# Kernel tuning notes

Hardware: AMD Instinct MI355X
Metric: run time of the kernel (lower is better)

## Reference

```python
import jax, jax.numpy as jnp
import numpy as np

B, L, D_IN, H, C = 64, 2048, 400, 200, 32
NEG = 1e12


def setup_inputs() -> dict:
    key = jax.random.key(0)
    k1, k2, k3, k4, k5 = jax.random.split(key, 5)
    x = jax.random.normal(k1, (B, L, D_IN), dtype=jnp.float32)
    category_bias = jax.random.normal(k2, (B, L, C), dtype=jnp.float32)
    att_mask = (jax.random.uniform(k3, (B, L)) > 0.2).astype(jnp.float32)
    # glorot-uniform-ish scales
    W_proj = jax.random.normal(k4, (D_IN, H), dtype=jnp.float32) * np.float32(np.sqrt(2.0 / (D_IN + H)))
    context = jax.random.normal(k5, (C, H), dtype=jnp.float32) * np.float32(np.sqrt(2.0 / (C + H)))
    lamada = jnp.zeros((1,), dtype=jnp.float32)
    return {"x": x, "category_bias": category_bias, "att_mask": att_mask,
            "W_proj": W_proj, "context": context, "lamada": lamada}


def reference(x, category_bias, att_mask, W_proj, context, lamada):
    # proj: [B, L, H] = tanh(x @ W_proj)  (Dense, no bias)
    proj = jnp.tanh(jnp.einsum("bld,dh->blh", x, W_proj))
    # scores vs learned context vectors: [B, L, C]
    weights = jnp.einsum("blh,ch->blc", proj, context) + lamada * category_bias
    # [B, C, L]
    weights = jnp.transpose(weights, (0, 2, 1))
    # additive large-negative mask, then softmax over sequence
    weights = weights - (1.0 - att_mask[:, None, :]) * NEG
    weights = jax.nn.softmax(weights, axis=-1)
    # poly representation: [B, C, D_IN]
    return jnp.einsum("bcl,bld->bcd", weights, x)
```

## Files before the change

kernel.cpp:

```cpp
#include <hip/hip_runtime.h>
#include <cmath>
#include <cstdint>

#define B_ 64
#define L_ 2048
#define DIN 400
#define H_ 200
#define C_ 32
#define NEGBIG 1e12f
#define KC1 13
#define NT1 13
#define KC2 7
#define MT2 2
#define NLC 16

typedef _Float16 half8 __attribute__((ext_vector_type(8)));
typedef float f32x4 __attribute__((ext_vector_type(4)));
typedef unsigned int uint4v __attribute__((ext_vector_type(4)));

__device__ __align__(16) _Float16 g_wfrag[KC1 * NT1 * 512];
__device__ __align__(16) _Float16 g_cfrag[KC2 * MT2 * 512];

static __device__ __forceinline__ f32x4 mfma16(half8 a, half8 b, f32x4 c) {
  return __builtin_amdgcn_mfma_f32_16x16x32_f16(a, b, c, 0, 0, 0);
}

static __device__ __forceinline__ float fast_tanh(float v) {
  const float e = __expf(2.0f * v);
  return 1.0f - 2.0f / (e + 1.0f);
}

__global__ __launch_bounds__(64) void k_prep(const float* __restrict__ Wp,
                                             const float* __restrict__ ctx)
{
  const int lane = threadIdx.x;
  const int bid = blockIdx.x;
  if (bid < KC1 * NT1) {
    const int q = bid / NT1, nt = bid % NT1;
    const int kb = q * 32 + (lane >> 4) * 8;
    const int n  = nt * 16 + (lane & 15);
    half8 h;
#pragma unroll
    for (int j = 0; j < 8; ++j) {
      const int k = kb + j;
      const float v = (k < DIN && n < H_) ? Wp[(size_t)k * H_ + n] : 0.0f;
      h[j] = (_Float16)v;
    }
    *reinterpret_cast<half8*>(&g_wfrag[((size_t)bid << 9) + (lane << 3)]) = h;
  } else {
    const int r = bid - KC1 * NT1;
    const int c  = (r % MT2) * 16 + (lane & 15);
    const int hb = (r / MT2) * 32 + (lane >> 4) * 8;
    half8 h;
#pragma unroll
    for (int j = 0; j < 8; ++j) {
      const int hh = hb + j;
      const float v = (hh < H_) ? ctx[(size_t)c * H_ + hh] : 0.0f;
      h[j] = (_Float16)v;
    }
    *reinterpret_cast<half8*>(&g_cfrag[((size_t)r << 9) + (lane << 3)]) = h;
  }
}

__global__ __launch_bounds__(256, 5) void k_scores(
    const float* __restrict__ x,
    const float* __restrict__ cb,
    const float* __restrict__ mask,
    const float* __restrict__ lam,
    float* __restrict__ S)
{
  __shared__ half8 smemv[1792];

  const int tid  = threadIdx.x;
  const int lane = tid & 63;
  const int w    = __builtin_amdgcn_readfirstlane(tid >> 6);
  const int b    = blockIdx.y;
  const int l0   = blockIdx.x * 64;
  const int oct  = lane >> 4;

  f32x4 acc[NT1];
#pragma unroll
  for (int nt = 0; nt < NT1; ++nt) acc[nt] = f32x4{0.f, 0.f, 0.f, 0.f};

  const float* xrow =
      x + ((size_t)b * L_ + l0 + w * 16 + (lane & 15)) * DIN + oct * 8;

  for (int i = w; i < NT1; i += 4) {
    const _Float16* gp = g_wfrag + (((size_t)i) << 9) + (lane << 3);
    __builtin_amdgcn_global_load_lds(
        (const __attribute__((address_space(1))) void*)gp,
        (__attribute__((address_space(3))) void*)(smemv + i * 64),
        16, 0, 0);
  }
  __builtin_amdgcn_sched_barrier(0);
  float4 cur0 = *reinterpret_cast<const float4*>(xrow);
  float4 cur1 = *reinterpret_cast<const float4*>(xrow + 4);

#pragma unroll
  for (int q = 0; q < KC1; ++q) {
    asm volatile("s_waitcnt vmcnt(2)\n\ts_barrier" ::: "memory");

    float4 nx0 = float4{0.f, 0.f, 0.f, 0.f};
    float4 nx1 = float4{0.f, 0.f, 0.f, 0.f};
    if (q < KC1 - 1) {
      const int nb = ((q + 1) & 1) * 832;
      for (int i = w; i < NT1; i += 4) {
        const _Float16* gp =
            g_wfrag + (((size_t)((q + 1) * NT1 + i)) << 9) + (lane << 3);
        __builtin_amdgcn_global_load_lds(
            (const __attribute__((address_space(1))) void*)gp,
            (__attribute__((address_space(3))) void*)(smemv + nb + i * 64),
            16, 0, 0);
      }
      __builtin_amdgcn_sched_barrier(0);
      const int k0 = (q + 1) * 32 + oct * 8;
      if (k0 + 7 < DIN) {
        nx0 = *reinterpret_cast<const float4*>(xrow + (q + 1) * 32);
        nx1 = *reinterpret_cast<const float4*>(xrow + (q + 1) * 32 + 4);
      }
    }

    float fa[8] = {cur0.x, cur0.y, cur0.z, cur0.w,
                   cur1.x, cur1.y, cur1.z, cur1.w};
    half8 ah;
#pragma unroll
    for (int j = 0; j < 8; ++j) ah[j] = (_Float16)fa[j];

    const int base = (q & 1) * 832;
#pragma unroll
    for (int nt = 0; nt < NT1; ++nt) {
      const half8 bh = smemv[base + nt * 64 + lane];
      acc[nt] = mfma16(ah, bh, acc[nt]);
    }
    cur0 = nx0;
    cur1 = nx1;
  }

  __syncthreads();
  if (lane >= 32) {
    half8 z = {};
    smemv[(24 + w) * 64 + lane] = z;
  }
  _Float16* Pp = reinterpret_cast<_Float16*>(smemv);
#pragma unroll
  for (int nt = 0; nt < NT1; ++nt) {
    const int h   = nt * 16 + (lane & 15);
    const int q2  = h >> 5;
    const int lpw = ((h >> 3) & 3) << 4;
    const int jj  = h & 7;
#pragma unroll
    for (int reg = 0; reg < 4; ++reg) {
      const int t = ((lane >> 4) << 2) + reg;
      const float p = fast_tanh(acc[nt][reg]);
      Pp[(size_t)(((q2 * 4 + w) * 64) + lpw + t) * 8 + jj] = (_Float16)p;
    }
  }

  f32x4 s0 = f32x4{0.f, 0.f, 0.f, 0.f};
  f32x4 s1 = f32x4{0.f, 0.f, 0.f, 0.f};
#pragma unroll
  for (int q2 = 0; q2 < KC2; ++q2) {
    const half8 pb = smemv[(q2 * 4 + w) * 64 + lane];
    const half8 c0 = *reinterpret_cast<const half8*>(
        g_cfrag + (((size_t)(q2 * 2)) << 9) + (lane << 3));
    const half8 c1 = *reinterpret_cast<const half8*>(
        g_cfrag + (((size_t)(q2 * 2 + 1)) << 9) + (lane << 3));
    s0 = mfma16(c0, pb, s0);
    s1 = mfma16(c1, pb, s1);
  }

  const int tok = (w << 4) | (lane & 15);
  const size_t bl = (size_t)b * L_ + l0 + tok;
  const float lamv = lam[0];
  const float mk = (1.0f - mask[bl]) * NEGBIG;
  const int cq = (lane >> 4) << 2;
  const float4 cb0 = *reinterpret_cast<const float4*>(cb + bl * C_ + cq);
  const float4 cb1 = *reinterpret_cast<const float4*>(cb + bl * C_ + 16 + cq);
  float* Sp = S + (size_t)b * C_ * L_ + l0 + tok;
  Sp[(size_t)(cq + 0) * L_] = s0[0] + lamv * cb0.x - mk;
  Sp[(size_t)(cq + 1) * L_] = s0[1] + lamv * cb0.y - mk;
  Sp[(size_t)(cq + 2) * L_] = s0[2] + lamv * cb0.z - mk;
  Sp[(size_t)(cq + 3) * L_] = s0[3] + lamv * cb0.w - mk;
  Sp[(size_t)(16 + cq + 0) * L_] = s1[0] + lamv * cb1.x - mk;
  Sp[(size_t)(16 + cq + 1) * L_] = s1[1] + lamv * cb1.y - mk;
  Sp[(size_t)(16 + cq + 2) * L_] = s1[2] + lamv * cb1.z - mk;
  Sp[(size_t)(16 + cq + 3) * L_] = s1[3] + lamv * cb1.w - mk;
}

__global__ __launch_bounds__(256) void k_softmax(float* __restrict__ S,
                                                 _Float16* __restrict__ wh)
{
  const int row = blockIdx.x;
  float* R = S + (size_t)row * L_;
  const int t8 = threadIdx.x * 8;

  const float4 va = *reinterpret_cast<const float4*>(R + t8);
  const float4 vb = *reinterpret_cast<const float4*>(R + t8 + 4);
  float v[8] = {va.x, va.y, va.z, va.w, vb.x, vb.y, vb.z, vb.w};
  float m = -3.4e38f;
#pragma unroll
  for (int j = 0; j < 8; ++j) m = fmaxf(m, v[j]);
#pragma unroll
  for (int o = 32; o > 0; o >>= 1) m = fmaxf(m, __shfl_xor(m, o));

  __shared__ float red[4];
  const int wid = threadIdx.x >> 6;
  if ((threadIdx.x & 63) == 0) red[wid] = m;
  __syncthreads();
  m = fmaxf(fmaxf(red[0], red[1]), fmaxf(red[2], red[3]));
  __syncthreads();

  float s = 0.f;
#pragma unroll
  for (int j = 0; j < 8; ++j) {
    v[j] = __expf(v[j] - m);
    s += v[j];
  }
#pragma unroll
  for (int o = 32; o > 0; o >>= 1) s += __shfl_xor(s, o);
  if ((threadIdx.x & 63) == 0) red[wid] = s;
  __syncthreads();
  s = red[0] + red[1] + red[2] + red[3];

  const float inv = 1.0f / s;
  if (wh != nullptr) {
    uint4v pk;
#pragma unroll
    for (int p = 0; p < 4; ++p) {
      const _Float16 h0 = (_Float16)(v[2 * p] * inv);
      const _Float16 h1 = (_Float16)(v[2 * p + 1] * inv);
      pk[p] = (unsigned int)__builtin_bit_cast(unsigned short, h0) |
              ((unsigned int)__builtin_bit_cast(unsigned short, h1) << 16);
    }
    *reinterpret_cast<uint4v*>(wh + (size_t)row * L_ + t8) = pk;
  } else {
    float4 oa = float4{v[0] * inv, v[1] * inv, v[2] * inv, v[3] * inv};
    float4 ob = float4{v[4] * inv, v[5] * inv, v[6] * inv, v[7] * inv};
    *reinterpret_cast<float4*>(R + t8) = oa;
    *reinterpret_cast<float4*>(R + t8 + 4) = ob;
  }
}

__global__ __launch_bounds__(512, 4) void k_out_mfma(
    const float* __restrict__ x,
    const _Float16* __restrict__ wh,
    _Float16* __restrict__ part)
{
  __shared__ unsigned int xsw[400 * 20];
  __shared__ unsigned int ws16[32][16];

  const int tid  = threadIdx.x;
  const int lane = tid & 63;
  const int w    = __builtin_amdgcn_readfirstlane(tid >> 6);
  const int b    = blockIdx.y;
  const int kq   = blockIdx.x;
  const int l0b  = kq * (L_ / NLC);

  const int ntile0 = (w < 7) ? w * 3 : 21;
  const int NTW    = (w < 7) ? 3 : 4;

  const int n   = lane & 15;
  const int oct = lane >> 4;

  f32x4 acc[4][2];
#pragma unroll
  for (int i = 0; i < 4; ++i) {
    acc[i][0] = f32x4{0.f, 0.f, 0.f, 0.f};
    acc[i][1] = f32x4{0.f, 0.f, 0.f, 0.f};
  }

  const float* xb = x + ((size_t)b * L_ + l0b) * DIN;
  const unsigned int* whb = reinterpret_cast<const unsigned int*>(
      wh + (size_t)b * C_ * L_ + l0b);

  float4 r0[4], r1[4];
  unsigned int wreg;

#pragma unroll
  for (int s = 0; s < 4; ++s) {
    const int i = s * 512 + tid;
    if (s < 3 || i < 1600) {
      const int lp = i / 100, qd = i - lp * 100;
      const float* src = xb + (size_t)(2 * lp) * DIN + 4 * qd;
      r0[s] = *reinterpret_cast<const float4*>(src);
      r1[s] = *reinterpret_cast<const float4*>(src + DIN);
    }
  }
  wreg = whb[((size_t)(tid >> 4) * L_) / 2 + (tid & 15)];

  const int NCH = (L_ / NLC) / 32;
  for (int ch = 0; ch < NCH; ++ch) {
    __syncthreads();

#pragma unroll
    for (int s = 0; s < 4; ++s) {
      const int i = s * 512 + tid;
      if (s < 3 || i < 1600) {
        const int lp = i / 100, qd = i - lp * 100;
#pragma unroll
        for (int k = 0; k < 4; ++k) {
          const int d = 4 * qd + k;
          const int sw = ((d >> 2) ^ (d >> 4)) & 3;
          const int col = (((lp >> 2) ^ sw) << 2) | (lp & 3);
          const _Float16 h0 = (_Float16)r0[s][k];
          const _Float16 h1 = (_Float16)r1[s][k];
          unsigned int pk = (unsigned int)__builtin_bit_cast(unsigned short, h0) |
                            ((unsigned int)__builtin_bit_cast(unsigned short, h1) << 16);
          xsw[d * 20 + col] = pk;
        }
      }
    }
    ws16[tid >> 4][tid & 15] = wreg;
    __syncthreads();

    if (ch + 1 < NCH) {
      const float* xc = xb + (size_t)((ch + 1) * 32) * DIN;
#pragma unroll
      for (int s = 0; s < 4; ++s) {
        const int i = s * 512 + tid;
        if (s < 3 || i < 1600) {
          const int lp = i / 100, qd = i - lp * 100;
          const float* src = xc + (size_t)(2 * lp) * DIN + 4 * qd;
          r0[s] = *reinterpret_cast<const float4*>(src);
          r1[s] = *reinterpret_cast<const float4*>(src + DIN);
        }
      }
      wreg = whb[((size_t)(tid >> 4) * L_ + (ch + 1) * 32) / 2 + (tid & 15)];
    }

    union { uint4v u; half8 h; } a0c, a1c;
    a0c.u = *reinterpret_cast<const uint4v*>(&ws16[n][oct * 4]);
    a1c.u = *reinterpret_cast<const uint4v*>(&ws16[n + 16][oct * 4]);
    const half8 a0 = a0c.h;
    const half8 a1 = a1c.h;

#pragma unroll
    for (int nt = 0; nt < 4; ++nt) {
      if (nt < NTW) {
        const int d0 = (ntile0 + nt) * 16 + n;
        const int sw = ((d0 >> 2) ^ (d0 >> 4)) & 3;
        const half8 bh = *reinterpret_cast<const half8*>(
            &xsw[d0 * 20 + ((oct ^ sw) << 2)]);
        acc[nt][0] = mfma16(a0, bh, acc[nt][0]);
        acc[nt][1] = mfma16(a1, bh, acc[nt][1]);
      }
    }
  }

  _Float16* pb = part + ((size_t)(b * NLC + kq) * C_) * DIN;
#pragma unroll
  for (int nt = 0; nt < 4; ++nt) {
    if (nt < NTW) {
      const int d = (ntile0 + nt) * 16 + n;
#pragma unroll
      for (int mt = 0; mt < 2; ++mt) {
#pragma unroll
        for (int reg = 0; reg < 4; ++reg) {
          const int c = mt * 16 + oct * 4 + reg;
          pb[(size_t)c * DIN + d] = (_Float16)acc[nt][mt][reg];
        }
      }
    }
  }
}

__global__ __launch_bounds__(256) void k_out_reduce(
    const _Float16* __restrict__ part, float* __restrict__ out)
{
  const int idx = blockIdx.x * 256 + threadIdx.x;
  const int per_b = C_ * DIN / 8;
  const int b = idx / per_b;
  const int r = idx - b * per_b;
  const uint4v* p = reinterpret_cast<const uint4v*>(part) +
                    (size_t)b * NLC * per_b + r;
  float s[8] = {};
#pragma unroll
  for (int lc = 0; lc < NLC; ++lc) {
    const uint4v v = p[(size_t)lc * per_b];
#pragma unroll
    for (int j = 0; j < 4; ++j) {
      s[2 * j]     += (float)__builtin_bit_cast(_Float16, (unsigned short)(v[j] & 0xffff));
      s[2 * j + 1] += (float)__builtin_bit_cast(_Float16, (unsigned short)(v[j] >> 16));
    }
  }
  float* o = out + (size_t)idx * 8;
  *reinterpret_cast<float4*>(o)     = float4{s[0], s[1], s[2], s[3]};
  *reinterpret_cast<float4*>(o + 4) = float4{s[4], s[5], s[6], s[7]};
}

__global__ __launch_bounds__(256) void k_out_atomic(
    const float* __restrict__ x,
    const float* __restrict__ Wt,
    float* __restrict__ out)
{
  __shared__ float ws_s[C_][256];
  const int tid  = threadIdx.x;
  const int b    = blockIdx.y;
  const int lc0  = blockIdx.x * 256;
  const int g    = __builtin_amdgcn_readfirstlane(tid >> 6);
  const int lane = tid & 63;

  {
    const int c  = tid >> 3;
    const int lb = (tid & 7) * 32;
    const float* src = Wt + ((size_t)b * C_ + c) * L_ + lc0 + lb;
#pragma unroll
    for (int j = 0; j < 32; j += 4)
      *reinterpret_cast<float4*>(&ws_s[c][lb + j]) =
          *reinterpret_cast<const float4*>(src + j);
  }
  __syncthreads();

  float a1[8][4] = {};
  float a2[8][4] = {};
  const bool has2 = lane < 36;
  const float* xb = x + ((size_t)b * L_ + lc0) * DIN;
  const int d1 = lane * 4;
  const int d2 = 256 + lane * 4;

  for (int l = 0; l < 256; ++l) {
    const float4 xv = *reinterpret_cast<const float4*>(xb + (size_t)l * DIN + d1);
    float4 xv2 = float4{0.f, 0.f, 0.f, 0.f};
    if (has2) xv2 = *reinterpret_cast<const float4*>(xb + (size_t)l * DIN + d2);
#pragma unroll
    for (int i = 0; i < 8; ++i) {
      const float wv = ws_s[g * 8 + i][l];
      a1[i][0] = fmaf(wv, xv.x, a1[i][0]);
      a1[i][1] = fmaf(wv, xv.y, a1[i][1]);
      a1[i][2] = fmaf(wv, xv.z, a1[i][2]);
      a1[i][3] = fmaf(wv, xv.w, a1[i][3]);
      a2[i][0] = fmaf(wv, xv2.x, a2[i][0]);
      a2[i][1] = fmaf(wv, xv2.y, a2[i][1]);
      a2[i][2] = fmaf(wv, xv2.z, a2[i][2]);
      a2[i][3] = fmaf(wv, xv2.w, a2[i][3]);
    }
  }

  float* ob = out + ((size_t)b * C_ + g * 8) * DIN;
#pragma unroll
  for (int i = 0; i < 8; ++i) {
#pragma unroll
    for (int kk = 0; kk < 4; ++kk)
      atomicAdd(ob + (size_t)i * DIN + d1 + kk, a1[i][kk]);
    if (has2) {
#pragma unroll
      for (int kk = 0; kk < 4; ++kk)
        atomicAdd(ob + (size_t)i * DIN + d2 + kk, a2[i][kk]);
    }
  }
}

extern "C" void kernel_launch(void* const* d_in, const int* in_sizes, int n_in,
                              void* d_out, int out_size, void* d_ws, size_t ws_size,
                              hipStream_t stream)
{
  const float* x    = (const float*)d_in[0];
  const float* cb   = (const float*)d_in[1];
  const float* mask = (const float*)d_in[2];
  const float* Wp   = (const float*)d_in[3];
  const float* ctx  = (const float*)d_in[4];
  const float* lam  = (const float*)d_in[5];
  float* out = (float*)d_out;

  const size_t part_bytes = (size_t)B_ * NLC * C_ * DIN * sizeof(_Float16);
  float* wsf  = (float*)d_ws;
  float* S    = wsf;
  _Float16* part = (_Float16*)d_ws;
  _Float16* wh = (_Float16*)((char*)d_ws + part_bytes);
  const size_t need = part_bytes +
                      (size_t)B_ * C_ * L_ * sizeof(_Float16);

  k_prep<<<dim3(KC1 * NT1 + KC2 * MT2), 64, 0, stream>>>(Wp, ctx);
  k_scores<<<dim3(L_ / 64, B_), 256, 0, stream>>>(x, cb, mask, lam, S);

  if (ws_size >= need) {
    k_softmax<<<dim3(B_ * C_), 256, 0, stream>>>(S, wh);
    k_out_mfma<<<dim3(NLC, B_), 512, 0, stream>>>(x, wh, part);
    k_out_reduce<<<dim3(B_ * C_ * DIN / 8 / 256), 256, 0, stream>>>(part, out);
  } else {
    k_softmax<<<dim3(B_ * C_), 256, 0, stream>>>(S, nullptr);
    hipMemsetAsync(d_out, 0, (size_t)out_size * sizeof(float), stream);
    k_out_atomic<<<dim3(L_ / 256, B_), 256, 0, stream>>>(x, S, out);
  }
}
```

Before: 104.7 us.

## Fuse scores, split-local softmax and weighted sum into one kernel with combine

A new k_fused kernel computes scores for a 64-token split and applies a split-local softmax (per-split max and denominator). It then multiplies the unnormalized probabilities with the block's x tile using MFMA, and writes fp16 partial outputs plus per-split stats. A k_combine kernel rescales and merges the 32 splits, flash-attention style. This removes the S round trip, the separate softmax pass and the second full read of x, but adds a large fp16 partial-output buffer and lower occupancy for the fused kernel. The atomic fallback path is dropped.

Result: no change. 102.7 us (-1.9%).

```diff
diff --git a/kernel.cpp b/kernel.cpp
--- a/kernel.cpp
+++ b/kernel.cpp
@@ -13,6 +13,7 @@
 #define KC2 7
 #define MT2 2
 #define NLC 16
+#define NS 32
 
 typedef _Float16 half8 __attribute__((ext_vector_type(8)));
 typedef float f32x4 __attribute__((ext_vector_type(4)));
@@ -62,20 +63,28 @@
   }
 }
 
-__global__ __launch_bounds__(256, 5) void k_scores(
+__global__ __launch_bounds__(256, 4) void k_fused(
     const float* __restrict__ x,
     const float* __restrict__ cb,
     const float* __restrict__ mask,
     const float* __restrict__ lam,
-    float* __restrict__ S)
-{
-  __shared__ half8 smemv[1792];
+    _Float16* __restrict__ O,
+    float* __restrict__ stats)
+{
+  __shared__ __align__(16) unsigned char shm[38144];
+  half8* smemv = reinterpret_cast<half8*>(shm);
+  unsigned int* xsw = reinterpret_cast<unsigned int*>(shm);
+  _Float16* Pl = reinterpret_cast<_Float16*>(shm + 32768);
+  float* redw  = reinterpret_cast<float*>(shm + 36864);
+  float* mfin  = reinterpret_cast<float*>(shm + 37376);
+  float* denf  = reinterpret_cast<float*>(shm + 37504);
 
   const int tid  = threadIdx.x;
   const int lane = tid & 63;
   const int w    = __builtin_amdgcn_readfirstlane(tid >> 6);
   const int b    = blockIdx.y;
-  const int l0   = blockIdx.x * 64;
+  const int split = blockIdx.x;
+  const int l0   = split * 64;
   const int oct  = lane >> 4;
 
   f32x4 acc[NT1];
@@ -169,6 +178,270 @@
     s1 = mfma16(c1, pb, s1);
   }
 
+  const int tok = (w << 4) | (lane & 15);
+  const size_t bl = (size_t)b * L_ + l0 + tok;
+  const float lamv = lam[0];
+  const float mk = (1.0f - mask[bl]) * NEGBIG;
+  const int cq = oct << 2;
+  const float4 cb0 = *reinterpret_cast<const float4*>(cb + bl * C_ + cq);
+  const float4 cb1 = *reinterpret_cast<const float4*>(cb + bl * C_ + 16 + cq);
+  float sv[8];
+  sv[0] = s0[0] + lamv * cb0.x - mk;  sv[1] = s0[1] + lamv * cb0.y - mk;
+  sv[2] = s0[2] + lamv * cb0.z - mk;  sv[3] = s0[3] + lamv * cb0.w - mk;
+  sv[4] = s1[0] + lamv * cb1.x - mk;  sv[5] = s1[1] + lamv * cb1.y - mk;
+  sv[6] = s1[2] + lamv * cb1.z - mk;  sv[7] = s1[3] + lamv * cb1.w - mk;
+  int cidx[8];
+#pragma unroll
+  for (int r = 0; r < 8; ++r) cidx[r] = (r < 4) ? (cq + r) : (16 + cq + r - 4);
+
+  float mx[8];
+#pragma unroll
+  for (int r = 0; r < 8; ++r) {
+    float v = sv[r];
+#pragma unroll
+    for (int off = 1; off < 16; off <<= 1) v = fmaxf(v, __shfl_xor(v, off));
+    mx[r] = v;
+  }
+  if ((lane & 15) == 0) {
+#pragma unroll
+    for (int r = 0; r < 8; ++r) redw[w * 32 + cidx[r]] = mx[r];
+  }
+  __syncthreads();
+  if (tid < 32)
+    mfin[tid] = fmaxf(fmaxf(redw[tid], redw[32 + tid]),
+                      fmaxf(redw[64 + tid], redw[96 + tid]));
+  __syncthreads();
+
+  float pd[8];
+#pragma unroll
+  for (int r = 0; r < 8; ++r) {
+    const float p = __expf(sv[r] - mfin[cidx[r]]);
+    pd[r] = p;
+    const int c = cidx[r];
+    Pl[c * 64 + ((((tok >> 3) ^ (c & 7))) << 3) + (tok & 7)] = (_Float16)p;
+  }
+#pragma unroll
+  for (int r = 0; r < 8; ++r) {
+    float v = pd[r];
+#pragma unroll
+    for (int off = 1; off < 16; off <<= 1) v += __shfl_xor(v, off);
+    pd[r] = v;
+  }
+  if ((lane & 15) == 0) {
+#pragma unroll
+    for (int r = 0; r < 8; ++r) redw[w * 32 + cidx[r]] = pd[r];
+  }
+  __syncthreads();
+  if (tid < 32)
+    denf[tid] = redw[tid] + redw[32 + tid] + redw[64 + tid] + redw[96 + tid];
+
+  const int ntile0w = (w == 0) ? 0 : (1 + 6 * w);
+  const int NTWv   = w ? 6 : 7;
+  const int n   = lane & 15;
+
+  f32x4 oacc[2][7];
+#pragma unroll
+  for (int ct = 0; ct < 2; ++ct)
+#pragma unroll
+    for (int nt = 0; nt < 7; ++nt) oacc[ct][nt] = f32x4{0.f, 0.f, 0.f, 0.f};
+
+  const float* xb = x + ((size_t)b * L_ + l0) * DIN;
+
+  for (int h = 0; h < 2; ++h) {
+    __syncthreads();
+    for (int s = 0; s < 7; ++s) {
+      const int i = s * 256 + tid;
+      if (i < 1600) {
+        const int lp = i / 100, qd = i - lp * 100;
+        const float* src = xb + (size_t)(h * 32 + 2 * lp) * DIN + 4 * qd;
+        const float4 r0 = *reinterpret_cast<const float4*>(src);
+        const float4 r1 = *reinterpret_cast<const float4*>(src + DIN);
+#pragma unroll
+        for (int k = 0; k < 4; ++k) {
+          const int d = 4 * qd + k;
+          const int sw = ((d >> 2) ^ (d >> 4)) & 3;
+          const int col = (((lp >> 2) ^ sw) << 2) | (lp & 3);
+          const _Float16 h0 = (_Float16)r0[k];
+          const _Float16 h1 = (_Float16)r1[k];
+          unsigned int pk = (unsigned int)__builtin_bit_cast(unsigned short, h0) |
+                            ((unsigned int)__builtin_bit_cast(unsigned short, h1) << 16);
+          xsw[d * 20 + col] = pk;
+        }
+      }
+    }
+    __syncthreads();
+
+    half8 aP[2];
+#pragma unroll
+    for (int ct = 0; ct < 2; ++ct) {
+      const int c = ct * 16 + n;
+      aP[ct] = *reinterpret_cast<const half8*>(
+          &Pl[c * 64 + ((((h << 2) | oct) ^ (c & 7)) << 3)]);
+    }
+#pragma unroll
+    for (int nt = 0; nt < 7; ++nt) {
+      if (nt < NTWv) {
+        const int d0 = (ntile0w + nt) * 16 + n;
+        const int sw = ((d0 >> 2) ^ (d0 >> 4)) & 3;
+        const half8 bh = *reinterpret_cast<const half8*>(
+            &xsw[d0 * 20 + ((oct ^ sw) << 2)]);
+        oacc[0][nt] = mfma16(aP[0], bh, oacc[0][nt]);
+        oacc[1][nt] = mfma16(aP[1], bh, oacc[1][nt]);
+      }
+    }
+  }
+
+  _Float16* Ob = O + ((size_t)(b * NS + split) * C_) * DIN;
+#pragma unroll
+  for (int nt = 0; nt < 7; ++nt) {
+    if (nt < NTWv) {
+      const int d = (ntile0w + nt) * 16 + n;
+#pragma unroll
+      for (int ct = 0; ct < 2; ++ct) {
+#pragma unroll
+        for (int reg = 0; reg < 4; ++reg) {
+          const int c = ct * 16 + oct * 4 + reg;
+          Ob[(size_t)c * DIN + d] = (_Float16)oacc[ct][nt][reg];
+        }
+      }
+    }
+  }
+  if (tid < 32) {
+    float* st = stats + (size_t)(b * NS + split) * 64;
+    st[tid]      = mfin[tid];
+    st[32 + tid] = denf[tid];
+  }
+}
+
+__global__ __launch_bounds__(256) void k_combine(
+    const _Float16* __restrict__ O, const float* __restrict__ stats,
+    float* __restrict__ out)
+{
+  const int idx = blockIdx.x * 256 + threadIdx.x;
+  const int b  = idx / (C_ * 50);
+  const int rm = idx - b * (C_ * 50);
+  const int c  = rm / 50;
+  const int dq = rm - c * 50;
+
+  const float* st = stats + (size_t)b * NS * 64;
+  float M = -3.4e38f;
+#pragma unroll
+  for (int s = 0; s < NS; ++s) M = fmaxf(M, st[s * 64 + c]);
+  float wsc[NS];
+  float denom = 0.f;
+#pragma unroll
+  for (int s = 0; s < NS; ++s) {
+    const float e = __expf(st[s * 64 + c] - M);
+    wsc[s] = e;
+    denom += e * st[s * 64 + 32 + c];
+  }
+  const float inv = 1.0f / denom;
+
+  float o[8] = {};
+  const uint4v* Op = reinterpret_cast<const uint4v*>(
+      O + ((size_t)(b * NS) * C_ + c) * DIN + dq * 8);
+#pragma unroll
+  for (int s = 0; s < NS; ++s) {
+    const uint4v v = Op[(size_t)s * (C_ * DIN / 8)];
+#pragma unroll
+    for (int j = 0; j < 4; ++j) {
+      o[2 * j]     += wsc[s] * (float)__builtin_bit_cast(_Float16, (unsigned short)(v[j] & 0xffff));
+      o[2 * j + 1] += wsc[s] * (float)__builtin_bit_cast(_Float16, (unsigned short)(v[j] >> 16));
+    }
+  }
+  float* op = out + ((size_t)(b * C_) + c) * DIN + dq * 8;
+  *reinterpret_cast<float4*>(op)     = float4{o[0]*inv, o[1]*inv, o[2]*inv, o[3]*inv};
+  *reinterpret_cast<float4*>(op + 4) = float4{o[4]*inv, o[5]*inv, o[6]*inv, o[7]*inv};
+}
+
+__global__ __launch_bounds__(256, 5) void k_scores(
+    const float* __restrict__ x, const float* __restrict__ cb,
+    const float* __restrict__ mask, const float* __restrict__ lam,
+    float* __restrict__ S)
+{
+  __shared__ half8 smemv[1792];
+  const int tid  = threadIdx.x;
+  const int lane = tid & 63;
+  const int w    = __builtin_amdgcn_readfirstlane(tid >> 6);
+  const int b    = blockIdx.y;
+  const int l0   = blockIdx.x * 64;
+  const int oct  = lane >> 4;
+
+  f32x4 acc[NT1];
+#pragma unroll
+  for (int nt = 0; nt < NT1; ++nt) acc[nt] = f32x4{0.f, 0.f, 0.f, 0.f};
+  const float* xrow =
+      x + ((size_t)b * L_ + l0 + w * 16 + (lane & 15)) * DIN + oct * 8;
+  for (int i = w; i < NT1; i += 4) {
+    const _Float16* gp = g_wfrag + (((size_t)i) << 9) + (lane << 3);
+    __builtin_amdgcn_global_load_lds(
+        (const __attribute__((address_space(1))) void*)gp,
+        (__attribute__((address_space(3))) void*)(smemv + i * 64), 16, 0, 0);
+  }
+  __builtin_amdgcn_sched_barrier(0);
+  float4 cur0 = *reinterpret_cast<const float4*>(xrow);
+  float4 cur1 = *reinterpret_cast<const float4*>(xrow + 4);
+#pragma unroll
+  for (int q = 0; q < KC1; ++q) {
+    asm volatile("s_waitcnt vmcnt(2)\n\ts_barrier" ::: "memory");
+    float4 nx0 = float4{0.f, 0.f, 0.f, 0.f};
+    float4 nx1 = float4{0.f, 0.f, 0.f, 0.f};
+    if (q < KC1 - 1) {
+      const int nb = ((q + 1) & 1) * 832;
+      for (int i = w; i < NT1; i += 4) {
+        const _Float16* gp =
+            g_wfrag + (((size_t)((q + 1) * NT1 + i)) << 9) + (lane << 3);
+        __builtin_amdgcn_global_load_lds(
+            (const __attribute__((address_space(1))) void*)gp,
+            (__attribute__((address_space(3))) void*)(smemv + nb + i * 64),
+            16, 0, 0);
+      }
+      __builtin_amdgcn_sched_barrier(0);
+      const int k0 = (q + 1) * 32 + oct * 8;
+      if (k0 + 7 < DIN) {
+        nx0 = *reinterpret_cast<const float4*>(xrow + (q + 1) * 32);
+        nx1 = *reinterpret_cast<const float4*>(xrow + (q + 1) * 32 + 4);
+      }
+    }
+    float fa[8] = {cur0.x, cur0.y, cur0.z, cur0.w,
+                   cur1.x, cur1.y, cur1.z, cur1.w};
+    half8 ah;
+#pragma unroll
+    for (int j = 0; j < 8; ++j) ah[j] = (_Float16)fa[j];
+    const int base = (q & 1) * 832;
+#pragma unroll
+    for (int nt = 0; nt < NT1; ++nt) {
+      const half8 bh = smemv[base + nt * 64 + lane];
+      acc[nt] = mfma16(ah, bh, acc[nt]);
+    }
+    cur0 = nx0; cur1 = nx1;
+  }
+  __syncthreads();
+  if (lane >= 32) { half8 z = {}; smemv[(24 + w) * 64 + lane] = z; }
+  _Float16* Pp = reinterpret_cast<_Float16*>(smemv);
+#pragma unroll
+  for (int nt = 0; nt < NT1; ++nt) {
+    const int h = nt * 16 + (lane & 15);
+    const int q2 = h >> 5, lpw = ((h >> 3) & 3) << 4, jj = h & 7;
+#pragma unroll
+    for (int reg = 0; reg < 4; ++reg) {
+      const int t = ((lane >> 4) << 2) + reg;
+      Pp[(size_t)(((q2 * 4 + w) * 64) + lpw + t) * 8 + jj] =
+          (_Float16)fast_tanh(acc[nt][reg]);
+    }
+  }
+  f32x4 s0 = f32x4{0.f, 0.f, 0.f, 0.f};
+  f32x4 s1 = f32x4{0.f, 0.f, 0.f, 0.f};
+#pragma unroll
+  for (int q2 = 0; q2 < KC2; ++q2) {
+    const half8 pb = smemv[(q2 * 4 + w) * 64 + lane];
+    const half8 c0 = *reinterpret_cast<const half8*>(
+        g_cfrag + (((size_t)(q2 * 2)) << 9) + (lane << 3));
+    const half8 c1 = *reinterpret_cast<const half8*>(
+        g_cfrag + (((size_t)(q2 * 2 + 1)) << 9) + (lane << 3));
+    s0 = mfma16(c0, pb, s0);
+    s1 = mfma16(c1, pb, s1);
+  }
   const int tok = (w << 4) | (lane & 15);
   const size_t bl = (size_t)b * L_ + l0 + tok;
   const float lamv = lam[0];
@@ -193,7 +466,6 @@
   const int row = blockIdx.x;
   float* R = S + (size_t)row * L_;
   const int t8 = threadIdx.x * 8;
-
   const float4 va = *reinterpret_cast<const float4*>(R + t8);
   const float4 vb = *reinterpret_cast<const float4*>(R + t8 + 4);
   float v[8] = {va.x, va.y, va.z, va.w, vb.x, vb.y, vb.z, vb.w};
@@ -202,26 +474,20 @@
   for (int j = 0; j < 8; ++j) m = fmaxf(m, v[j]);
 #pragma unroll
   for (int o = 32; o > 0; o >>= 1) m = fmaxf(m, __shfl_xor(m, o));
-
   __shared__ float red[4];
   const int wid = threadIdx.x >> 6;
   if ((threadIdx.x & 63) == 0) red[wid] = m;
   __syncthreads();
   m = fmaxf(fmaxf(red[0], red[1]), fmaxf(red[2], red[3]));
   __syncthreads();
-
   float s = 0.f;
 #pragma unroll
-  for (int j = 0; j < 8; ++j) {
-    v[j] = __expf(v[j] - m);
-    s += v[j];
-  }
+  for (int j = 0; j < 8; ++j) { v[j] = __expf(v[j] - m); s += v[j]; }
 #pragma unroll
   for (int o = 32; o > 0; o >>= 1) s += __shfl_xor(s, o);
   if ((threadIdx.x & 63) == 0) red[wid] = s;
   __syncthreads();
   s = red[0] + red[1] + red[2] + red[3];
-
   const float inv = 1.0f / s;
   if (wh != nullptr) {
     uint4v pk;
@@ -234,48 +500,38 @@
     }
     *reinterpret_cast<uint4v*>(wh + (size_t)row * L_ + t8) = pk;
   } else {
-    float4 oa = float4{v[0] * inv, v[1] * inv, v[2] * inv, v[3] * inv};
-    float4 ob = float4{v[4] * inv, v[5] * inv, v[6] * inv, v[7] * inv};
-    *reinterpret_cast<float4*>(R + t8) = oa;
-    *reinterpret_cast<float4*>(R + t8 + 4) = ob;
+#pragma unroll
+    for (int j = 0; j < 8; ++j) R[t8 + j] = v[j] * inv;
   }
 }
 
 __global__ __launch_bounds__(512, 4) void k_out_mfma(
-    const float* __restrict__ x,
-    const _Float16* __restrict__ wh,
+    const float* __restrict__ x, const _Float16* __restrict__ wh,
     _Float16* __restrict__ part)
 {
   __shared__ unsigned int xsw[400 * 20];
   __shared__ unsigned int ws16[32][16];
-
   const int tid  = threadIdx.x;
   const int lane = tid & 63;
   const int w    = __builtin_amdgcn_readfirstlane(tid >> 6);
   const int b    = blockIdx.y;
   const int kq   = blockIdx.x;
   const int l0b  = kq * (L_ / NLC);
-
   const int ntile0 = (w < 7) ? w * 3 : 21;
   const int NTW    = (w < 7) ? 3 : 4;
-
   const int n   = lane & 15;
   const int oct = lane >> 4;
-
   f32x4 acc[4][2];
 #pragma unroll
   for (int i = 0; i < 4; ++i) {
     acc[i][0] = f32x4{0.f, 0.f, 0.f, 0.f};
     acc[i][1] = f32x4{0.f, 0.f, 0.f, 0.f};
   }
-
   const float* xb = x + ((size_t)b * L_ + l0b) * DIN;
   const unsigned int* whb = reinterpret_cast<const unsigned int*>(
       wh + (size_t)b * C_ * L_ + l0b);
-
   float4 r0[4], r1[4];
   unsigned int wreg;
-
 #pragma unroll
   for (int s = 0; s < 4; ++s) {
     const int i = s * 512 + tid;
@@ -287,11 +543,9 @@
     }
   }
   wreg = whb[((size_t)(tid >> 4) * L_) / 2 + (tid & 15)];
-
   const int NCH = (L_ / NLC) / 32;
   for (int ch = 0; ch < NCH; ++ch) {
     __syncthreads();
-
 #pragma unroll
     for (int s = 0; s < 4; ++s) {
       const int i = s * 512 + tid;
@@ -312,7 +566,6 @@
     }
     ws16[tid >> 4][tid & 15] = wreg;
     __syncthreads();
-
     if (ch + 1 < NCH) {
       const float* xc = xb + (size_t)((ch + 1) * 32) * DIN;
 #pragma unroll
@@ -327,13 +580,11 @@
       }
       wreg = whb[((size_t)(tid >> 4) * L_ + (ch + 1) * 32) / 2 + (tid & 15)];
     }
-
     union { uint4v u; half8 h; } a0c, a1c;
     a0c.u = *reinterpret_cast<const uint4v*>(&ws16[n][oct * 4]);
     a1c.u = *reinterpret_cast<const uint4v*>(&ws16[n + 16][oct * 4]);
     const half8 a0 = a0c.h;
     const half8 a1 = a1c.h;
-
 #pragma unroll
     for (int nt = 0; nt < 4; ++nt) {
       if (nt < NTW) {
@@ -346,7 +597,6 @@
       }
     }
   }
-
   _Float16* pb = part + ((size_t)(b * NLC + kq) * C_) * DIN;
 #pragma unroll
   for (int nt = 0; nt < 4; ++nt) {
@@ -388,68 +638,6 @@
   *reinterpret_cast<float4*>(o + 4) = float4{s[4], s[5], s[6], s[7]};
 }
 
-__global__ __launch_bounds__(256) void k_out_atomic(
-    const float* __restrict__ x,
-    const float* __restrict__ Wt,
-    float* __restrict__ out)
-{
-  __shared__ float ws_s[C_][256];
-  const int tid  = threadIdx.x;
-  const int b    = blockIdx.y;
-  const int lc0  = blockIdx.x * 256;
-  const int g    = __builtin_amdgcn_readfirstlane(tid >> 6);
-  const int lane = tid & 63;
-
-  {
-    const int c  = tid >> 3;
-    const int lb = (tid & 7) * 32;
-    const float* src = Wt + ((size_t)b * C_ + c) * L_ + lc0 + lb;
-#pragma unroll
-    for (int j = 0; j < 32; j += 4)
-      *reinterpret_cast<float4*>(&ws_s[c][lb + j]) =
-          *reinterpret_cast<const float4*>(src + j);
-  }
-  __syncthreads();
-
-  float a1[8][4] = {};
-  float a2[8][4] = {};
-  const bool has2 = lane < 36;
-  const float* xb = x + ((size_t)b * L_ + lc0) * DIN;
-  const int d1 = lane * 4;
-  const int d2 = 256 + lane * 4;
-
-  for (int l = 0; l < 256; ++l) {
-    const float4 xv = *reinterpret_cast<const float4*>(xb + (size_t)l * DIN + d1);
-    float4 xv2 = float4{0.f, 0.f, 0.f, 0.f};
-    if (has2) xv2 = *reinterpret_cast<const float4*>(xb + (size_t)l * DIN + d2);
-#pragma unroll
-    for (int i = 0; i < 8; ++i) {
-      const float wv = ws_s[g * 8 + i][l];
-      a1[i][0] = fmaf(wv, xv.x, a1[i][0]);
-      a1[i][1] = fmaf(wv, xv.y, a1[i][1]);
-      a1[i][2] = fmaf(wv, xv.z, a1[i][2]);
-      a1[i][3] = fmaf(wv, xv.w, a1[i][3]);
-      a2[i][0] = fmaf(wv, xv2.x, a2[i][0]);
-      a2[i][1] = fmaf(wv, xv2.y, a2[i][1]);
-      a2[i][2] = fmaf(wv, xv2.z, a2[i][2]);
-      a2[i][3] = fmaf(wv, xv2.w, a2[i][3]);
-    }
-  }
-
-  float* ob = out + ((size_t)b * C_ + g * 8) * DIN;
-#pragma unroll
-  for (int i = 0; i < 8; ++i) {
-#pragma unroll
-    for (int kk = 0; kk < 4; ++kk)
-      atomicAdd(ob + (size_t)i * DIN + d1 + kk, a1[i][kk]);
-    if (has2) {
-#pragma unroll
-      for (int kk = 0; kk < 4; ++kk)
-        atomicAdd(ob + (size_t)i * DIN + d2 + kk, a2[i][kk]);
-    }
-  }
-}
-
 extern "C" void kernel_launch(void* const* d_in, const int* in_sizes, int n_in,
                               void* d_out, int out_size, void* d_ws, size_t ws_size,
                               hipStream_t stream)
@@ -462,24 +650,24 @@
   const float* lam  = (const float*)d_in[5];
   float* out = (float*)d_out;
 
+  k_prep<<<dim3(KC1 * NT1 + KC2 * MT2), 64, 0, stream>>>(Wp, ctx);
+
+  const size_t O_bytes = (size_t)B_ * NS * C_ * DIN * sizeof(_Float16);
+  const size_t st_bytes = (size_t)B_ * NS * 64 * sizeof(float);
+  if (ws_size >= O_bytes + st_bytes) {
+    _Float16* O = (_Float16*)d_ws;
+    float* stats = (float*)((char*)d_ws + O_bytes);
+    k_fused<<<dim3(NS, B_), 256, 0, stream>>>(x, cb, mask, lam, O, stats);
+    k_combine<<<dim3(B_ * C_ * 50 / 256), 256, 0, stream>>>(O, stats, out);
+    return;
+  }
+
   const size_t part_bytes = (size_t)B_ * NLC * C_ * DIN * sizeof(_Float16);
-  float* wsf  = (float*)d_ws;
-  float* S    = wsf;
+  float* S = (float*)d_ws;
   _Float16* part = (_Float16*)d_ws;
   _Float16* wh = (_Float16*)((char*)d_ws + part_bytes);
-  const size_t need = part_bytes +
-                      (size_t)B_ * C_ * L_ * sizeof(_Float16);
-
-  k_prep<<<dim3(KC1 * NT1 + KC2 * MT2), 64, 0, stream>>>(Wp, ctx);
   k_scores<<<dim3(L_ / 64, B_), 256, 0, stream>>>(x, cb, mask, lam, S);
-
-  if (ws_size >= need) {
-    k_softmax<<<dim3(B_ * C_), 256, 0, stream>>>(S, wh);
-    k_out_mfma<<<dim3(NLC, B_), 512, 0, stream>>>(x, wh, part);
-    k_out_reduce<<<dim3(B_ * C_ * DIN / 8 / 256), 256, 0, stream>>>(part, out);
-  } else {
-    k_softmax<<<dim3(B_ * C_), 256, 0, stream>>>(S, nullptr);
-    hipMemsetAsync(d_out, 0, (size_t)out_size * sizeof(float), stream);
-    k_out_atomic<<<dim3(L_ / 256, B_), 256, 0, stream>>>(x, S, out);
-  }
-}
+  k_softmax<<<dim3(B_ * C_), 256, 0, stream>>>(S, wh);
+  k_out_mfma<<<dim3(NLC, B_), 512, 0, stream>>>(x, wh, part);
+  k_out_reduce<<<dim3(B_ * C_ * DIN / 8 / 256), 256, 0, stream>>>(part, out);
+}
```
